# Optimization experiments

Hardware: AMD Instinct MI355X
Metric: run time of the kernel (lower is better)

Reference implementation:

```python
import jax, jax.numpy as jnp
import numpy as np

B, N_CHANS, T = 128, 64, 1000
SPATIAL_EXP, SPATIAL_MERGE = 240, 32
FILTERS = [41, 51, 61]
TEMP_EXP = 2
BASE = 2
FEATURE_DIM = [(SPATIAL_EXP // (N_CHANS - BASE**i + 1), BASE**i)
               for i in range(2, 6) if BASE**i < N_CHANS] + [(SPATIAL_EXP, N_CHANS)]
SUM_SP = sum(d0 * (N_CHANS - d1 + 1) for d0, d1 in FEATURE_DIM)   # 1078
N_FEAT = len(FILTERS) * TEMP_EXP * SPATIAL_MERGE                  # 192
FC_IN = (N_FEAT + 1) * N_FEAT // 2                                # 18528
N_CLASS = 4
BN_EPS = 1e-5


def _conv2d(x, w, b, groups=1, pad_w=0):
    y = jax.lax.conv_general_dilated(
        x, w, (1, 1), ((0, 0), (pad_w, pad_w)),
        dimension_numbers=('NCHW', 'OIHW', 'NCHW'),
        feature_group_count=groups)
    return y + b[None, :, None, None]


def _bn(x, gamma, beta):
    # inference-mode BatchNorm2d with running_mean=0, running_var=1
    return gamma[None, :, None, None] * x * (1.0 / np.sqrt(1.0 + BN_EPS)) + beta[None, :, None, None]


def setup_inputs() -> dict:
    key = jax.random.key(0)
    ks = iter(jax.random.split(key, 40))
    inp = {"x": jax.random.normal(next(ks), (B, N_CHANS, T), jnp.float32)}
    for i, (d0, d1) in enumerate(FEATURE_DIM):
        inp[f"sw{i}"] = jax.random.normal(next(ks), (d0, 1, d1, 1), jnp.float32) / np.sqrt(d1)
        inp[f"sb{i}"] = jnp.zeros((d0,), jnp.float32)
    inp["mw"] = jax.random.normal(next(ks), (SPATIAL_MERGE, 1, SUM_SP, 1), jnp.float32) / np.sqrt(SUM_SP)
    inp["mb"] = jnp.zeros((SPATIAL_MERGE,), jnp.float32)
    inp["mg"] = jnp.ones((SPATIAL_MERGE,), jnp.float32)
    inp["mbt"] = jnp.zeros((SPATIAL_MERGE,), jnp.float32)
    for i, size in enumerate(FILTERS):
        co = TEMP_EXP * SPATIAL_MERGE
        inp[f"tw{i}"] = jax.random.normal(next(ks), (co, 1, 1, size), jnp.float32) / np.sqrt(size)
        inp[f"tb{i}"] = jnp.zeros((co,), jnp.float32)
        inp[f"tg{i}"] = jnp.ones((co,), jnp.float32)
        inp[f"tbt{i}"] = jnp.zeros((co,), jnp.float32)
    inp["fcw"] = jax.random.normal(next(ks), (N_CLASS, FC_IN), jnp.float32) / np.sqrt(FC_IN)
    inp["fcb"] = jnp.zeros((N_CLASS,), jnp.float32)
    return inp


def reference(x, sw0, sb0, sw1, sb1, sw2, sb2, sw3, sb3, sw4, sb4,
              mw, mb, mg, mbt,
              tw0, tb0, tg0, tbt0, tw1, tb1, tg1, tbt1, tw2, tb2, tg2, tbt2,
              fcw, fcb):
    b, _, t = x.shape
    xi = x[:, None]                                        # (B,1,C,T)
    sp = [(sw0, sb0), (sw1, sb1), (sw2, sb2), (sw3, sb3), (sw4, sb4)]
    feats = [_conv2d(xi, w, bb).reshape(b, -1, t) for w, bb in sp]
    Xs = jnp.concatenate(feats, 1)[:, None]                # (B,1,1078,T)
    Xs = _bn(_conv2d(Xs, mw, mb), mg, mbt)                 # (B,32,1,T)
    tp = [(tw0, tb0, tg0, tbt0), (tw1, tb1, tg1, tbt1), (tw2, tb2, tg2, tbt2)]
    Xt = jnp.stack([_bn(_conv2d(Xs, w, bb, groups=SPATIAL_MERGE, pad_w=w.shape[-1] // 2), g, bt)
                    for w, bb, g, bt in tp], 1)            # (B,3,64,1,T)
    Xt = Xt.reshape(b, -1, t)                              # (B,192,T)
    Xb = jnp.einsum('bct,bdt->bcd', Xt, Xt) / (t - 1)      # Gram matrix (B,192,192)
    L = jnp.linalg.cholesky(Xb)
    n = L.shape[-1]
    rows, cols = np.tril_indices(n, -1)                    # row-major: matches torch per-row concat
    diag = jnp.diagonal(L, axis1=1, axis2=2)               # (B,192)
    tangent = jnp.concatenate([jnp.log(diag), L[:, rows, cols]], axis=1)  # (B,18528)
    return tangent @ fcw.T + fcb
```

## Files before the change

### kernel.cpp

```cpp
#include <hip/hip_runtime.h>
#include <hip/hip_bf16.h>
#include <math.h>


#define A_OFF    0
#define BETA_OFF 2048
#define TBE_OFF  2080
#define TWE_OFF  2304
#define XS_OFF   14592
#define XBP_OFF  4110592
#define XT_OFF   7256320
#define WS_NEED  ((size_t)19839232 * 4)

#define SBN 0.9999950000374997f

typedef short short8 __attribute__((ext_vector_type(8)));
typedef float floatx4 __attribute__((ext_vector_type(4)));

__device__ __forceinline__ unsigned short f2bf(float f) {
    unsigned u = __float_as_uint(f);
    u += 0x7FFFu + ((u >> 16) & 1u);
    return (unsigned short)(u >> 16);
}
__device__ __forceinline__ float bf2f(unsigned short h) {
    return __uint_as_float(((unsigned)h) << 16);
}

__global__ __launch_bounds__(256) void prep_kernel(
    const float* __restrict__ sw0, const float* __restrict__ sw1,
    const float* __restrict__ sw2, const float* __restrict__ sw3,
    const float* __restrict__ sw4,
    const float* __restrict__ sb0, const float* __restrict__ sb1,
    const float* __restrict__ sb2, const float* __restrict__ sb3,
    const float* __restrict__ sb4,
    const float* __restrict__ mw, const float* __restrict__ mb,
    const float* __restrict__ mg, const float* __restrict__ mbt,
    const float* __restrict__ tw0, const float* __restrict__ tw1,
    const float* __restrict__ tw2,
    const float* __restrict__ tb0, const float* __restrict__ tb1,
    const float* __restrict__ tb2,
    const float* __restrict__ tg0, const float* __restrict__ tg1,
    const float* __restrict__ tg2,
    const float* __restrict__ tbt0, const float* __restrict__ tbt1,
    const float* __restrict__ tbt2,
    float* __restrict__ ws)
{
    const float* tws[3]  = {tw0, tw1, tw2};
    const float* tbs[3]  = {tb0, tb1, tb2};
    const float* tgs[3]  = {tg0, tg1, tg2};
    const float* tbts[3] = {tbt0, tbt1, tbt2};
    const int fsz[3] = {41, 51, 61};

    int gid = blockIdx.x * 256 + threadIdx.x;
    int gw = gid >> 6, lane = gid & 63;

    if (gw < 2048) {
        int m = gw >> 6, c = gw & 63;
        float acc = 0.f;
        for (int j = lane; j < 1078; j += 64) {
            float wv = mw[m * 1078 + j];
            float sv = 0.f;
            if (j < 183) {
                int r = j, fq = r / 61, h = r - fq * 61, k = c - h;
                if (k >= 0 && k < 4)  sv = sw0[fq * 4 + k];
            } else if (j < 411) {
                int r = j - 183, fq = r / 57, h = r - fq * 57, k = c - h;
                if (k >= 0 && k < 8)  sv = sw1[fq * 8 + k];
            } else if (j < 607) {
                int r = j - 411, fq = r / 49, h = r - fq * 49, k = c - h;
                if (k >= 0 && k < 16) sv = sw2[fq * 16 + k];
            } else if (j < 838) {
                int r = j - 607, fq = r / 33, h = r - fq * 33, k = c - h;
                if (k >= 0 && k < 32) sv = sw3[fq * 32 + k];
            } else {
                int r = j - 838;
                sv = sw4[r * 64 + c];
            }
            acc += wv * sv;
        }
        for (int off = 32; off > 0; off >>= 1) acc += __shfl_down(acc, off);
        if (lane == 0) ws[A_OFF + m * 64 + c] = mg[m] * SBN * acc;
    } else if (gw < 2080) {
        int m = gw - 2048;
        float acc = 0.f;
        for (int j = lane; j < 1078; j += 64) {
            float wv = mw[m * 1078 + j];
            float sv;
            if (j < 183)      sv = sb0[j / 61];
            else if (j < 411) sv = sb1[(j - 183) / 57];
            else if (j < 607) sv = sb2[(j - 411) / 49];
            else if (j < 838) sv = sb3[(j - 607) / 33];
            else              sv = sb4[j - 838];
            acc += wv * sv;
        }
        for (int off = 32; off > 0; off >>= 1) acc += __shfl_down(acc, off);
        if (lane == 0)
            ws[BETA_OFF + m] = mg[m] * SBN * (acc + mb[m]) + mbt[m];
    } else {
        int id2 = gid - 133120;
        if (id2 < 0) return;
        if (id2 < 192) {
            int fi = id2 >> 6, o = id2 & 63;
            ws[TBE_OFF + id2] = tgs[fi][o] * SBN * tbs[fi][o] + tbts[fi][o];
        } else if (id2 < 12480) {
            int idx = id2 - 192;
            int fi = idx >> 12, r = idx & 4095, o = r >> 6, k = r & 63;
            int sz = fsz[fi];
            float v = 0.f;
            if (k < sz) v = tgs[fi][o] * SBN * tws[fi][o * sz + k];
            ws[TWE_OFF + idx] = v;
        }
    }
}

__global__ __launch_bounds__(256) void xs_kernel(const float* __restrict__ x,
                                                 float* __restrict__ ws)
{
    __shared__ float Ash[2048];
    __shared__ float Bsh[32];
    int tid = threadIdx.x;
    for (int i = tid; i < 2048; i += 256) Ash[i] = ws[A_OFF + i];
    if (tid < 32) Bsh[tid] = ws[BETA_OFF + tid];
    __syncthreads();

    int gid = blockIdx.x * 256 + tid;
    int b = gid / 1000, t = gid - b * 1000;
    const float* xp = x + b * 64000 + t;

    float acc[32];
#pragma unroll
    for (int m = 0; m < 32; ++m) acc[m] = Bsh[m];
#pragma unroll 4
    for (int c = 0; c < 64; ++c) {
        float xv = xp[c * 1000];
#pragma unroll
        for (int m = 0; m < 32; ++m) acc[m] += Ash[m * 64 + c] * xv;
    }
    float* op = ws + XS_OFF + b * 32000 + t;
#pragma unroll
    for (int m = 0; m < 32; ++m) op[m * 1000] = acc[m];
}

__device__ __forceinline__ void conv8_vals(float* __restrict__ a,
                                           const float* __restrict__ xp,
                                           const unsigned short* __restrict__ wp,
                                           int szp, float bias)
{
    float xw[8];
#pragma unroll
    for (int i = 0; i < 8; ++i) { a[i] = bias; xw[i] = xp[i]; }
    for (int k = 0; k < szp; k += 8) {
#pragma unroll
        for (int p = 0; p < 8; ++p) {
            float w = bf2f(wp[(k + p) * 64]);
#pragma unroll
            for (int i = 0; i < 8; ++i) a[i] += w * xw[(p + i) & 7];
            xw[p] = xp[k + p + 8];
        }
    }
}

template<int SZP>
__device__ __forceinline__ void conv16(float* __restrict__ a,
                                       const float* __restrict__ xp,
                                       const unsigned int* __restrict__ w2o,
                                       float bias)
{
    float xw[16];
#pragma unroll
    for (int i = 0; i < 16; ++i) { a[i] = bias; xw[i] = xp[i]; }
#pragma unroll
    for (int k = 0; k < SZP; k += 8) {
#pragma unroll
        for (int p = 0; p < 8; ++p) {
            unsigned int u = w2o[((k + p) >> 1) * 64];
            float w = ((p & 1) == 0) ? __uint_as_float(u << 16)
                                     : __uint_as_float(u & 0xffff0000u);
#pragma unroll
            for (int i = 0; i < 16; ++i)
                a[i] += w * xw[(k + p + i) & 15];
            xw[(k + p) & 15] = xp[k + p + 16];
        }
    }
}

template<int SZP, int BASE>
__device__ __forceinline__ void xt_task(const float* __restrict__ xp0,
                                        const unsigned int* __restrict__ w2o,
                                        float bias,
                                        unsigned short* __restrict__ op,
                                        int tbase)
{
#pragma unroll 1
    for (int s = 0; s < 4; ++s) {
        float a[16];
        conv16<SZP>(a, xp0 + s * 16 + BASE, w2o, bias);
#pragma unroll
        for (int half = 0; half < 2; ++half) {
            short8 hv;
#pragma unroll
            for (int i = 0; i < 8; ++i) {
                int gt = tbase + s * 16 + half * 8 + i;
                hv[i] = (short)((gt < 1000) ? f2bf(a[half * 8 + i]) : 0);
            }
            *(short8*)&op[s * 16 + half * 8] = hv;
        }
    }
}

__global__ __launch_bounds__(384) void xt_kernel(float* __restrict__ ws)
{
    __shared__ float xs_sh[32 * 201];
    __shared__ unsigned int tw2_sh[5376];
    __shared__ float tb_sh[192];

    int tid = threadIdx.x;
    int wg = blockIdx.x;
    int b = wg >> 3, chunk = wg & 7;
    int t0 = chunk * 128;

    for (int idx = tid; idx < 5376; idx += 384) {
        int bank, rem;
        if (idx < 1536)      { bank = 0; rem = idx; }
        else if (idx < 3328) { bank = 1; rem = idx - 1536; }
        else                 { bank = 2; rem = idx - 3328; }
        int kt2 = rem >> 6, o = rem & 63;
        unsigned int lo = f2bf(ws[TWE_OFF + bank * 4096 + o * 64 + 2 * kt2]);
        unsigned int hi = f2bf(ws[TWE_OFF + bank * 4096 + o * 64 + 2 * kt2 + 1]);
        tw2_sh[idx] = lo | (hi << 16);
    }
    if (tid < 192) tb_sh[tid] = ws[TBE_OFF + tid];

    const float* xsrow = ws + XS_OFF + b * 32000;
    for (int idx = tid; idx < 6400; idx += 384) {
        int m = idx / 200, q = idx - m * 200;
        int gt = t0 - 30 + q;
        xs_sh[m * 201 + q] = (gt >= 0 && gt < 1000) ? xsrow[m * 1000 + gt] : 0.f;
    }
    __syncthreads();

    unsigned short* xtg = (unsigned short*)(ws + XT_OFF);
    const int lane = tid & 63;
    const int wv   = tid >> 6;
    const int bank = wv % 3, thalf = wv / 3;
    const int o = lane, m = o >> 1;
    const int ch = bank * 64 + o;
    float bias = tb_sh[ch];
    int tbase = t0 + thalf * 64;
    unsigned short* op = &xtg[(size_t)(b * 192 + ch) * 1024 + tbase];
    const float* xp0 = &xs_sh[m * 201 + thalf * 64];

    if (bank == 0)      xt_task<48, 10>(xp0, &tw2_sh[0]    + o, bias, op, tbase);
    else if (bank == 1) xt_task<56, 5>( xp0, &tw2_sh[1536] + o, bias, op, tbase);
    else                xt_task<64, 0>( xp0, &tw2_sh[3328] + o, bias, op, tbase);
}

__global__ __launch_bounds__(512) void gram_kernel(float* __restrict__ ws)
{
    __shared__ __align__(16) unsigned short xsh[192 * 136];

    int tid = threadIdx.x;
    int b = blockIdx.x >> 1, h = blockIdx.x & 1;
    int nrows = h ? 192 : 128;

    const unsigned short* xtg = (const unsigned short*)(ws + XT_OFF);
    const unsigned short* gb = xtg + (size_t)b * 192 * 1024;

    floatx4 acc[3][2];
#pragma unroll
    for (int t = 0; t < 3; ++t)
#pragma unroll
        for (int sjl = 0; sjl < 2; ++sjl) acc[t][sjl] = (floatx4){0.f, 0.f, 0.f, 0.f};

    const int lane = tid & 63;
    const int wv8  = tid >> 6;
    const int wvr  = wv8 & 3;
    const int sjb  = (wv8 >> 2) * 2;
    const int m15  = lane & 15;
    const int quad = lane >> 4;
    int nloads = nrows * 16;

    for (int t0 = 0; t0 < 1024; t0 += 128) {
        for (int idx = tid; idx < nloads; idx += 512) {
            int row = idx >> 4, c8 = idx & 15;
            *(short8*)&xsh[row * 136 + c8 * 8] =
                *(const short8*)&gb[(size_t)row * 1024 + t0 + c8 * 8];
        }
        __syncthreads();
        if (h == 0) {
#pragma unroll
            for (int k0 = 0; k0 < 128; k0 += 32) {
                short8 a0 = *(const short8*)&xsh[(      wvr * 16 + m15) * 136 + quad * 8 + k0];
                short8 a1 = *(const short8*)&xsh[( 64 + wvr * 16 + m15) * 136 + quad * 8 + k0];
#pragma unroll
                for (int sjl = 0; sjl < 2; ++sjl) {
                    int sj = sjb + sjl;
                    short8 b0 = *(const short8*)&xsh[(      sj * 16 + m15) * 136 + quad * 8 + k0];
                    short8 b1 = *(const short8*)&xsh[( 64 + sj * 16 + m15) * 136 + quad * 8 + k0];
                    acc[0][sjl] = __builtin_amdgcn_mfma_f32_16x16x32_bf16(a0, b0, acc[0][sjl], 0, 0, 0);
                    acc[1][sjl] = __builtin_amdgcn_mfma_f32_16x16x32_bf16(a1, b0, acc[1][sjl], 0, 0, 0);
                    acc[2][sjl] = __builtin_amdgcn_mfma_f32_16x16x32_bf16(a1, b1, acc[2][sjl], 0, 0, 0);
                }
            }
        } else {
#pragma unroll
            for (int k0 = 0; k0 < 128; k0 += 32) {
                short8 a2 = *(const short8*)&xsh[(128 + wvr * 16 + m15) * 136 + quad * 8 + k0];
#pragma unroll
                for (int sjl = 0; sjl < 2; ++sjl) {
                    int sj = sjb + sjl;
                    short8 b0 = *(const short8*)&xsh[(      sj * 16 + m15) * 136 + quad * 8 + k0];
                    short8 b1 = *(const short8*)&xsh[( 64 + sj * 16 + m15) * 136 + quad * 8 + k0];
                    short8 b2 = *(const short8*)&xsh[(128 + sj * 16 + m15) * 136 + quad * 8 + k0];
                    acc[0][sjl] = __builtin_amdgcn_mfma_f32_16x16x32_bf16(a2, b0, acc[0][sjl], 0, 0, 0);
                    acc[1][sjl] = __builtin_amdgcn_mfma_f32_16x16x32_bf16(a2, b1, acc[1][sjl], 0, 0, 0);
                    acc[2][sjl] = __builtin_amdgcn_mfma_f32_16x16x32_bf16(a2, b2, acc[2][sjl], 0, 0, 0);
                }
            }
        }
        __syncthreads();
    }

    const float sc = 1.0f / 999.0f;
#pragma unroll
    for (int t = 0; t < 3; ++t) {
        int tileid = h ? (3 + t) : t;
        float* xbp = ws + XBP_OFF + b * 24576 + tileid * 4096;
#pragma unroll
        for (int sjl = 0; sjl < 2; ++sjl)
#pragma unroll
            for (int r = 0; r < 4; ++r) {
                int i = wvr * 16 + quad * 4 + r;
                int j = (sjb + sjl) * 16 + m15;
                xbp[i * 64 + j] = acc[t][sjl][r] * sc;
            }
    }
}

__global__ __launch_bounds__(256, 3) void cov_kernel(float* __restrict__ ws)
{
    __shared__ float xs_sh[32 * 129];
    __shared__ __align__(16) unsigned short xt_sh[2 * 64 * 72];
    __shared__ unsigned short tw_sh[120 * 64];
    __shared__ float tb_sh[128];

    int tid = threadIdx.x;
    int wg = blockIdx.x;
    int b = wg / 6, tile = wg - b * 6;
    const int TIa[6] = {0, 1, 1, 2, 2, 2};
    const int TJa[6] = {0, 0, 1, 0, 1, 2};
    int I = TIa[tile], J = TJa[tile];
    const int fpad[3] = {20, 25, 30};
    const int fszp[3] = {48, 56, 64};
    int padI = fpad[I], szpI = fszp[I];
    int padJ = fpad[J], szpJ = fszp[J];
    bool diag = (I == J);

    int nI = szpI * 64;
    for (int idx = tid; idx < nI; idx += 256) {
        int kt = idx >> 6, o = idx & 63;
        tw_sh[idx] = f2bf(ws[TWE_OFF + I * 4096 + o * 64 + kt]);
    }
    if (!diag) {
        int nJ = szpJ * 64;
        for (int idx = tid; idx < nJ; idx += 256) {
            int kt = idx >> 6, o = idx & 63;
            tw_sh[nI + idx] = f2bf(ws[TWE_OFF + J * 4096 + o * 64 + kt]);
        }
    }
    if (tid < 64)        tb_sh[tid] = ws[TBE_OFF + I * 64 + tid];
    else if (tid < 128)  tb_sh[tid] = ws[TBE_OFF + J * 64 + (tid - 64)];

    floatx4 acc[4];
#pragma unroll
    for (int sj = 0; sj < 4; ++sj) acc[sj] = (floatx4){0.f, 0.f, 0.f, 0.f};

    const float* xsrow = ws + XS_OFF + b * 32000;
    unsigned short* xtI = xt_sh;
    unsigned short* xtJ = diag ? xt_sh : (xt_sh + 64 * 72);

    const int lane = tid & 63;
    const int wv   = tid >> 6;
    const int m15  = lane & 15;
    const int quad = lane >> 4;

    for (int t0 = 0; t0 < 1000; t0 += 64) {
        for (int idx = tid; idx < 4096; idx += 256) {
            int m = idx >> 7, q = idx & 127;
            int gt = t0 - 30 + q;
            xs_sh[m * 129 + q] = (gt >= 0 && gt < 1000) ? xsrow[m * 1000 + gt] : 0.f;
        }
        __syncthreads();
        for (int it = 0; it < 2; ++it) {
            int o   = lane;
            int grp = wv + it * 4;
            int tlb = grp * 8;
            int m   = o >> 1;
            float a[8];
            conv8_vals(a, &xs_sh[m * 129 + tlb + (30 - padI)], &tw_sh[o],
                       szpI, tb_sh[o]);
            short8 hv;
#pragma unroll
            for (int i = 0; i < 8; ++i) {
                int gt = t0 + tlb + i;
                hv[i] = (short)((gt < 1000) ? f2bf(a[i]) : 0);
            }
            *(short8*)&xtI[o * 72 + tlb] = hv;
            if (!diag) {
                conv8_vals(a, &xs_sh[m * 129 + tlb + (30 - padJ)], &tw_sh[nI + o],
                           szpJ, tb_sh[64 + o]);
#pragma unroll
                for (int i = 0; i < 8; ++i) {
                    int gt = t0 + tlb + i;
                    hv[i] = (short)((gt < 1000) ? f2bf(a[i]) : 0);
                }
                *(short8*)&xtJ[o * 72 + tlb] = hv;
            }
        }
        __syncthreads();
        const unsigned short* ap = &xtI[(wv * 16 + m15) * 72 + quad * 8];
#pragma unroll
        for (int k0 = 0; k0 < 64; k0 += 32) {
            short8 af = *(const short8*)(ap + k0);
#pragma unroll
            for (int sj = 0; sj < 4; ++sj) {
                short8 bf = *(const short8*)&xtJ[(sj * 16 + m15) * 72 + quad * 8 + k0];
                acc[sj] = __builtin_amdgcn_mfma_f32_16x16x32_bf16(af, bf, acc[sj],
                                                                  0, 0, 0);
            }
        }
        __syncthreads();
    }

    float* xbp = ws + XBP_OFF + b * 24576 + tile * 4096;
    const float sc = 1.0f / 999.0f;
#pragma unroll
    for (int sj = 0; sj < 4; ++sj)
#pragma unroll
        for (int r = 0; r < 4; ++r) {
            int i = wv * 16 + quad * 4 + r;
            int j = sj * 16 + m15;
            xbp[i * 64 + j] = acc[sj][r] * sc;
        }
}

#define LSTR 196
__device__ __forceinline__ int lidx(int i, int c) {
    return i * LSTR + ((((c >> 2) ^ ((i >> 3) & 7)) << 2) | (c & 3));
}

__device__ __forceinline__ void diag16(float* Lm, int j0, int i,
                                       float* invd_sh)
{
    float r[16];
#pragma unroll
    for (int c = 0; c < 16; ++c) r[c] = Lm[lidx(j0 + i, j0 + c)];
#pragma unroll
    for (int jj = 0; jj < 16; ++jj) {
        float d = __shfl(r[jj], jj);
        d = fmaxf(d, 1e-20f);
        float s = sqrtf(d);
        float inv = 1.0f / s;
        if (i == jj) { r[jj] = s; invd_sh[jj] = inv; }
        else if (i > jj) r[jj] *= inv;
#pragma unroll
        for (int cc = jj + 1; cc < 16; ++cc) {
            float vc = __shfl(r[jj], cc);
            if (i >= cc) r[cc] -= r[jj] * vc;
        }
    }
#pragma unroll
    for (int c = 0; c < 16; ++c)
        if (c <= i) Lm[lidx(j0 + i, j0 + c)] = r[c];
}

__global__ __launch_bounds__(512) void chol_kernel(const float* __restrict__ ws,
                                                   const float* __restrict__ fcw,
                                                   const float* __restrict__ fcb,
                                                   float* __restrict__ out)
{
    __shared__ __align__(16) float L[192 * LSTR];
    __shared__ float invd_sh[16];
    __shared__ float red[8][4];

    int b = blockIdx.x, tid = threadIdx.x;
    const float* Xb = ws + XBP_OFF + b * 24576;
    const int TIa[6] = {0, 1, 1, 2, 2, 2};
    const int TJa[6] = {0, 0, 1, 0, 1, 2};

    for (int idx = tid; idx < 6144; idx += 512) {
        int fi = idx << 2;
        int t = fi >> 12, r = (fi >> 6) & 63, c = fi & 63;
        floatx4 val = *(const floatx4*)&Xb[fi];
        *(floatx4*)&L[lidx(TIa[t] * 64 + r, TJa[t] * 64 + c)] = val;
    }
    __syncthreads();

    if (tid < 16) diag16(L, 0, tid, invd_sh);
    __syncthreads();

    for (int p = 0; p <= 10; ++p) {
        int j0 = p * 16, j1 = j0 + 16;

        {
            int i = j1 + tid;
            if (i < 192) {
                floatx4 vv[4];
#pragma unroll
                for (int q = 0; q < 4; ++q)
                    vv[q] = *(floatx4*)&L[lidx(i, j0 + 4 * q)];
                float v[16];
#pragma unroll
                for (int k = 0; k < 16; ++k) v[k] = vv[k >> 2][k & 3];
#pragma unroll
                for (int k = 0; k < 16; ++k) {
                    float vk = v[k];
#pragma unroll
                    for (int p2 = 0; p2 < k; ++p2)
                        vk -= v[p2] * L[lidx(j0 + k, j0 + p2)];
                    v[k] = vk * invd_sh[k];
                }
#pragma unroll
                for (int k = 0; k < 16; ++k) vv[k >> 2][k & 3] = v[k];
#pragma unroll
                for (int q = 0; q < 4; ++q)
                    *(floatx4*)&L[lidx(i, j0 + 4 * q)] = vv[q];
            }
        }
        __syncthreads();

        int RT = (192 - j1) >> 3;
        int nt = RT * RT + RT;
        if (tid < 64) {
            int r = tid & 15, cq = tid >> 4;
            floatx4 a4 = *(floatx4*)&L[lidx(j1 + r, j1 + cq * 4)];
#pragma unroll
            for (int k = 0; k < 16; ++k) {
                float pr = L[lidx(j1 + r, j0 + k)];
#pragma unroll
                for (int cc = 0; cc < 4; ++cc)
                    a4[cc] -= pr * L[lidx(j1 + cq * 4 + cc, j0 + k)];
            }
            *(floatx4*)&L[lidx(j1 + r, j1 + cq * 4)] = a4;
            if (tid < 16) diag16(L, j1, tid, invd_sh);
        } else {
            for (int t = 6 + (tid - 64); t < nt; t += 448) {
                int ti = (int)(sqrtf((float)t + 0.25f) - 0.5f);
                while (ti * ti + ti > t) --ti;
                while ((ti + 1) * (ti + 1) + (ti + 1) <= t) ++ti;
                int tj = t - ti * ti - ti;
                int i0 = j1 + 8 * ti, c0 = j1 + 4 * tj;
                floatx4 a[8];
#pragma unroll
                for (int r = 0; r < 8; ++r)
                    a[r] = *(floatx4*)&L[lidx(i0 + r, c0)];
#pragma unroll 1
                for (int kk = 0; kk < 16; kk += 4) {
                    floatx4 pi[8], pc[4];
#pragma unroll
                    for (int r = 0; r < 8; ++r)
                        pi[r] = *(floatx4*)&L[lidx(i0 + r, j0 + kk)];
#pragma unroll
                    for (int c = 0; c < 4; ++c)
                        pc[c] = *(floatx4*)&L[lidx(c0 + c, j0 + kk)];
#pragma unroll
                    for (int k = 0; k < 4; ++k)
#pragma unroll
                        for (int r = 0; r < 8; ++r) {
                            float ar = pi[r][k];
#pragma unroll
                            for (int c = 0; c < 4; ++c)
                                a[r][c] -= ar * pc[c][k];
                        }
                }
#pragma unroll
                for (int r = 0; r < 8; ++r)
                    *(floatx4*)&L[lidx(i0 + r, c0)] = a[r];
            }
        }
        __syncthreads();
    }

    float a0 = 0.f, a1 = 0.f, a2 = 0.f, a3 = 0.f;
    for (int d = tid; d < 192; d += 512) {
        float v = logf(fmaxf(L[lidx(d, d)], 1e-30f));
        a0 += v * fcw[d];
        a1 += v * fcw[18528 + d];
        a2 += v * fcw[2 * 18528 + d];
        a3 += v * fcw[3 * 18528 + d];
    }
    {
        int e = tid;
        float fe = (float)e;
        int r = (int)((1.0f + sqrtf(1.0f + 8.0f * fe)) * 0.5f);
        if (r < 1) r = 1;
        while (r * (r - 1) / 2 > e) --r;
        while ((r + 1) * r / 2 <= e) ++r;
        int c = e - r * (r - 1) / 2;
        for (; e < 18336; e += 512) {
            float v = L[lidx(r, c)];
            int dd = 192 + e;
            a0 += v * fcw[dd];
            a1 += v * fcw[18528 + dd];
            a2 += v * fcw[2 * 18528 + dd];
            a3 += v * fcw[3 * 18528 + dd];
            c += 512;
            while (c >= r) { c -= r; ++r; }
        }
    }
    for (int off = 32; off > 0; off >>= 1) {
        a0 += __shfl_down(a0, off);
        a1 += __shfl_down(a1, off);
        a2 += __shfl_down(a2, off);
        a3 += __shfl_down(a3, off);
    }
    int wv = tid >> 6, ln = tid & 63;
    if (ln == 0) { red[wv][0] = a0; red[wv][1] = a1; red[wv][2] = a2; red[wv][3] = a3; }
    __syncthreads();
    if (tid < 4) {
        float s = red[0][tid] + red[1][tid] + red[2][tid] + red[3][tid]
                + red[4][tid] + red[5][tid] + red[6][tid] + red[7][tid]
                + fcb[tid];
        out[b * 4 + tid] = s;
    }
}

extern "C" void kernel_launch(void* const* d_in, const int* in_sizes, int n_in,
                              void* d_out, int out_size, void* d_ws, size_t ws_size,
                              hipStream_t stream)
{
    float* ws = (float*)d_ws;

    prep_kernel<<<569, 256, 0, stream>>>(
        (const float*)d_in[1], (const float*)d_in[3], (const float*)d_in[5],
        (const float*)d_in[7], (const float*)d_in[9],
        (const float*)d_in[2], (const float*)d_in[4], (const float*)d_in[6],
        (const float*)d_in[8], (const float*)d_in[10],
        (const float*)d_in[11], (const float*)d_in[12], (const float*)d_in[13],
        (const float*)d_in[14],
        (const float*)d_in[15], (const float*)d_in[19], (const float*)d_in[23],
        (const float*)d_in[16], (const float*)d_in[20], (const float*)d_in[24],
        (const float*)d_in[17], (const float*)d_in[21], (const float*)d_in[25],
        (const float*)d_in[18], (const float*)d_in[22], (const float*)d_in[26], ws);
    xs_kernel<<<500, 256, 0, stream>>>((const float*)d_in[0], ws);
    if (ws_size >= WS_NEED) {
        xt_kernel<<<1024, 384, 0, stream>>>(ws);
        gram_kernel<<<256, 512, 0, stream>>>(ws);
    } else {
        cov_kernel<<<768, 256, 0, stream>>>(ws);
    }
    chol_kernel<<<128, 512, 0, stream>>>(ws, (const float*)d_in[27],
                                         (const float*)d_in[28], (float*)d_out);
}
```

Before: 344.7 us.

## Fuse spatial projection into temporal conv kernel, dropping xs_kernel launch

```diff
diff --git a/kernel.cpp b/kernel.cpp
--- a/kernel.cpp
+++ b/kernel.cpp
@@ -208,17 +208,22 @@
     }
 }
 
-__global__ __launch_bounds__(384) void xt_kernel(float* __restrict__ ws)
+__global__ __launch_bounds__(384) void xt_kernel(const float* __restrict__ x,
+                                                 float* __restrict__ ws)
 {
     __shared__ float xs_sh[32 * 201];
     __shared__ unsigned int tw2_sh[5376];
     __shared__ float tb_sh[192];
+    __shared__ float Ash[2048];
+    __shared__ float Bsh[32];
 
     int tid = threadIdx.x;
     int wg = blockIdx.x;
     int b = wg >> 3, chunk = wg & 7;
     int t0 = chunk * 128;
 
+    for (int i = tid; i < 2048; i += 384) Ash[i] = ws[A_OFF + i];
+    if (tid < 32) Bsh[tid] = ws[BETA_OFF + tid];
     for (int idx = tid; idx < 5376; idx += 384) {
         int bank, rem;
         if (idx < 1536)      { bank = 0; rem = idx; }
@@ -230,12 +235,28 @@
         tw2_sh[idx] = lo | (hi << 16);
     }
     if (tid < 192) tb_sh[tid] = ws[TBE_OFF + tid];
-
-    const float* xsrow = ws + XS_OFF + b * 32000;
-    for (int idx = tid; idx < 6400; idx += 384) {
-        int m = idx / 200, q = idx - m * 200;
+    __syncthreads();
+
+    if (tid < 200) {
+        int q = tid;
         int gt = t0 - 30 + q;
-        xs_sh[m * 201 + q] = (gt >= 0 && gt < 1000) ? xsrow[m * 1000 + gt] : 0.f;
+        float acc[32];
+        if (gt >= 0 && gt < 1000) {
+            const float* xp = x + b * 64000 + gt;
+#pragma unroll
+            for (int m = 0; m < 32; ++m) acc[m] = Bsh[m];
+#pragma unroll 4
+            for (int c = 0; c < 64; ++c) {
+                float xv = xp[c * 1000];
+#pragma unroll
+                for (int m = 0; m < 32; ++m) acc[m] += Ash[m * 64 + c] * xv;
+            }
+        } else {
+#pragma unroll
+            for (int m = 0; m < 32; ++m) acc[m] = 0.f;
+        }
+#pragma unroll
+        for (int m = 0; m < 32; ++m) xs_sh[m * 201 + q] = acc[m];
     }
     __syncthreads();
 
@@ -642,11 +663,11 @@
         (const float*)d_in[16], (const float*)d_in[20], (const float*)d_in[24],
         (const float*)d_in[17], (const float*)d_in[21], (const float*)d_in[25],
         (const float*)d_in[18], (const float*)d_in[22], (const float*)d_in[26], ws);
-    xs_kernel<<<500, 256, 0, stream>>>((const float*)d_in[0], ws);
     if (ws_size >= WS_NEED) {
-        xt_kernel<<<1024, 384, 0, stream>>>(ws);
+        xt_kernel<<<1024, 384, 0, stream>>>((const float*)d_in[0], ws);
         gram_kernel<<<256, 512, 0, stream>>>(ws);
     } else {
+        xs_kernel<<<500, 256, 0, stream>>>((const float*)d_in[0], ws);
         cov_kernel<<<768, 256, 0, stream>>>(ws);
     }
     chol_kernel<<<128, 512, 0, stream>>>(ws, (const float*)d_in[27],
```

Measured after the change: 339.5 us (median of 3 runs). Within noise of the previous version (-1.5%).
